# Performance work log

Hardware: AMD Instinct MI355X
Metric: run time of the kernel (lower is better)

Reference implementation:

```python
import jax, jax.numpy as jnp
import numpy as np

N = 50000      # nodes
E = 800000     # edges (before self loops)
EMB = 128      # input feature dim
HID = 32       # per-head hidden dim
HEADS = 4      # gat1 heads
G = 64         # graphs in batch
NEG_SLOPE = 0.2


def setup_inputs() -> dict:
    key = jax.random.key(0)
    ks = jax.random.split(key, 14)
    glorot = lambda k, shape, fan: (jax.random.normal(k, shape) / np.sqrt(fan)).astype(jnp.float32)
    x = jax.random.normal(ks[0], (N, EMB), dtype=jnp.float32)
    edge_index = jax.random.randint(ks[1], (2, E), 0, N, dtype=jnp.int64)
    batch = jnp.sort(jax.random.randint(ks[2], (N,), 0, G, dtype=jnp.int64))
    return {
        "x": x,
        "edge_index": edge_index,
        "batch": batch,
        # GATConv 1: EMB -> HID per head, HEADS heads, concat
        "W1": glorot(ks[3], (EMB, HEADS * HID), EMB),
        "att_src1": glorot(ks[4], (HEADS, HID), HID),
        "att_dst1": glorot(ks[5], (HEADS, HID), HID),
        "b1": jnp.zeros((HEADS * HID,), jnp.float32),
        # GATConv 2: HEADS*HID -> HID, 1 head
        "W2": glorot(ks[6], (HEADS * HID, HID), HEADS * HID),
        "att_src2": glorot(ks[7], (1, HID), HID),
        "att_dst2": glorot(ks[8], (1, HID), HID),
        "b2": jnp.zeros((HID,), jnp.float32),
        # attentional pooling gate MLP: Linear(HID,HID)->ReLU->Linear(HID,1)
        "g_w1": glorot(ks[9], (HID, HID), HID),
        "g_b1": jnp.zeros((HID,), jnp.float32),
        "g_w2": glorot(ks[10], (HID, 1), HID),
        "g_b2": jnp.zeros((1,), jnp.float32),
    }


def _gat(x, W, att_src, att_dst, bias, src, dst, heads, out_dim):
    """PyG-style GATConv with precomputed self-looped (src, dst)."""
    n = x.shape[0]
    h = (x @ W).reshape(n, heads, out_dim)              # [N, H, C]
    a_src = (h * att_src).sum(-1)                       # [N, H]
    a_dst = (h * att_dst).sum(-1)                       # [N, H]
    e = jax.nn.leaky_relu(a_src[src] + a_dst[dst], NEG_SLOPE)   # [Etot, H]
    # segment softmax over incoming edges of each dst node
    m = jax.ops.segment_max(e, dst, num_segments=n)
    ex = jnp.exp(e - m[dst])
    denom = jax.ops.segment_sum(ex, dst, num_segments=n)
    alpha = ex / (denom[dst] + 1e-16)                   # [Etot, H]
    out = jax.ops.segment_sum(alpha[:, :, None] * h[src], dst, num_segments=n)
    return out.reshape(n, heads * out_dim) + bias


def reference(x, edge_index, batch, W1, att_src1, att_dst1, b1,
              W2, att_src2, att_dst2, b2, g_w1, g_b1, g_w2, g_b2):
    n = x.shape[0]
    loops = jnp.arange(n, dtype=edge_index.dtype)
    src = jnp.concatenate([edge_index[0], loops])       # add_self_loops=True
    dst = jnp.concatenate([edge_index[1], loops])
    h = jax.nn.elu(_gat(x, W1, att_src1, att_dst1, b1, src, dst, HEADS, HID))
    h = jax.nn.elu(_gat(h, W2, att_src2, att_dst2, b2, src, dst, 1, HID))
    # attentional aggregation per graph
    gate = jax.nn.relu(h @ g_w1 + g_b1) @ g_w2 + g_b2   # [N, 1]
    gm = jax.ops.segment_max(gate, batch, num_segments=G)
    ge = jnp.exp(gate - gm[batch])
    gs = jax.ops.segment_sum(ge, batch, num_segments=G)
    w = ge / (gs[batch] + 1e-16)
    return jax.ops.segment_sum(w * h, batch, num_segments=G)  # [G, HID]
```

## Files before the change

kernel.cpp:

```cpp
#include <hip/hip_runtime.h>
#include <hip/hip_bf16.h>

#define NEG_SLOPE 0.2f
#define BW  128
#define BSH 7

__device__ __forceinline__ float elu1f(float v) {
    return v > 0.f ? v : expm1f(v);
}
__device__ __forceinline__ float bf2f(ushort u) {
    return __uint_as_float(((unsigned)u) << 16);
}
__device__ __forceinline__ ushort f2bf(float f) {
    return __bfloat16_as_ushort(__float2bfloat16(f));
}
__device__ __forceinline__ unsigned fflip(float f) {
    unsigned u = __float_as_uint(f);
    return (u & 0x80000000u) ? ~u : (u | 0x80000000u);
}
__device__ __forceinline__ float funflip(unsigned u) {
    u = (u & 0x80000000u) ? (u & 0x7FFFFFFFu) : ~u;
    return __uint_as_float(u);
}

__global__ __launch_bounds__(256) void k_bcount(
    const int* __restrict__ ei, int E, int Et, int nbk, int* __restrict__ bcnt)
{
    __shared__ int h[512];
    for (int i = threadIdx.x; i < nbk; i += 256) h[i] = 0;
    __syncthreads();
    const int start = blockIdx.x * 4096;
    const int end   = min(start + 4096, Et);
    for (int i = start + threadIdx.x; i < end; i += 256) {
        int d = (i < E) ? ei[E + i] : i - E;
        atomicAdd(&h[d >> BSH], 1);
    }
    __syncthreads();
    for (int i = threadIdx.x; i < nbk; i += 256)
        if (h[i]) atomicAdd(&bcnt[i], h[i]);
}

__global__ __launch_bounds__(512) void k_bscan(
    const int* __restrict__ bcnt, int nbk, int Et,
    int* __restrict__ bbase, int* __restrict__ bcur,
    const int* __restrict__ batch, int* __restrict__ gbound, int N, int G)
{
    __shared__ int s[512];
    int v = (threadIdx.x < nbk) ? bcnt[threadIdx.x] : 0;
    s[threadIdx.x] = v;
    __syncthreads();
#pragma unroll
    for (int off = 1; off < 512; off <<= 1) {
        int t = (threadIdx.x >= off) ? s[threadIdx.x - off] : 0;
        __syncthreads();
        s[threadIdx.x] += t;
        __syncthreads();
    }
    if (threadIdx.x < nbk) {
        int ex = s[threadIdx.x] - v;
        bbase[threadIdx.x] = ex;
        bcur[threadIdx.x]  = ex;
    }
    if (threadIdx.x == 0) bbase[nbk] = Et;
    if (threadIdx.x <= (unsigned)G) {
        int target = threadIdx.x;
        int lo = 0, hi = N;
        while (lo < hi) { int mid = (lo + hi) >> 1; if (batch[mid] < target) lo = mid + 1; else hi = mid; }
        gbound[threadIdx.x] = lo;
    }
}

__global__ __launch_bounds__(256) void k_bscatter(
    const int* __restrict__ ei, int E, int Et, int nbk,
    int* __restrict__ bcur, unsigned* __restrict__ ebuk)
{
    __shared__ int h[512];
    __shared__ int cur[512];
    for (int i = threadIdx.x; i < nbk; i += 256) h[i] = 0;
    __syncthreads();
    const int start = blockIdx.x * 4096;
    const int end   = min(start + 4096, Et);
    for (int i = start + threadIdx.x; i < end; i += 256) {
        int d = (i < E) ? ei[E + i] : i - E;
        atomicAdd(&h[d >> BSH], 1);
    }
    __syncthreads();
    for (int i = threadIdx.x; i < nbk; i += 256)
        cur[i] = h[i] ? atomicAdd(&bcur[i], h[i]) : 0;
    __syncthreads();
    for (int i = start + threadIdx.x; i < end; i += 256) {
        int s, d;
        if (i < E) { s = ei[i]; d = ei[E + i]; } else { s = i - E; d = s; }
        int p = atomicAdd(&cur[d >> BSH], 1);
        ebuk[p] = ((unsigned)(d & (BW - 1)) << 25) | (unsigned)s;
    }
}

__global__ __launch_bounds__(256) void k_csr(
    const unsigned* __restrict__ ebuk, const int* __restrict__ bbase,
    int N, int Et, int* __restrict__ rowp, int* __restrict__ esrc)
{
    const int b = blockIdx.x;
    __shared__ int cnt[BW];
    __shared__ int pre[BW];
    __shared__ int lcur[BW];
    if (threadIdx.x < BW) cnt[threadIdx.x] = 0;
    __syncthreads();
    const int e0 = bbase[b], e1 = bbase[b + 1];
    for (int i = e0 + threadIdx.x; i < e1; i += 256)
        atomicAdd(&cnt[ebuk[i] >> 25], 1);
    __syncthreads();
    if (threadIdx.x < BW) pre[threadIdx.x] = cnt[threadIdx.x];
    __syncthreads();
#pragma unroll
    for (int off = 1; off < BW; off <<= 1) {
        int v = (threadIdx.x < BW && threadIdx.x >= off) ? pre[threadIdx.x - off] : 0;
        __syncthreads();
        if (threadIdx.x < BW) pre[threadIdx.x] += v;
        __syncthreads();
    }
    const int d0 = b << BSH;
    if (threadIdx.x < BW) {
        int r = e0 + pre[threadIdx.x] - cnt[threadIdx.x];
        int d = d0 + threadIdx.x;
        if (d < N) rowp[d] = r;
        lcur[threadIdx.x] = r;
    }
    if (b == 0 && threadIdx.x == 0) rowp[N] = Et;
    __syncthreads();
    for (int i = e0 + threadIdx.x; i < e1; i += 256) {
        unsigned e = ebuk[i];
        int p = atomicAdd(&lcur[e >> 25], 1);
        esrc[p] = (int)(e & 0x1FFFFFFu);
    }
}

__global__ __launch_bounds__(256) void k_gemm1(
    const float* __restrict__ x, const float* __restrict__ W,
    const float* __restrict__ att_s, const float* __restrict__ att_d,
    ushort* __restrict__ h1, float* __restrict__ asT, float* __restrict__ ad1,
    unsigned* __restrict__ gmaxu, int N)
{
    __shared__ __align__(16) float sW[16][128];
    __shared__ __align__(16) float sX[32][16];
    __shared__ unsigned smax[4];
    const int t  = threadIdx.x;
    const int c4 = t & 31;
    const int rg = t >> 5;
    const int row0 = blockIdx.x * 32;
    const float4* W4 = (const float4*)W;

    if (t < 4) smax[t] = 0;

    float4 acc[4];
#pragma unroll
    for (int i = 0; i < 4; i++) acc[i] = {0.f, 0.f, 0.f, 0.f};

    for (int k0 = 0; k0 < 128; k0 += 16) {
        __syncthreads();
#pragma unroll
        for (int j = 0; j < 2; j++) {
            int idx = j * 256 + t;
            int r = idx >> 5, cc = idx & 31;
            *(float4*)&sW[r][cc * 4] = W4[(k0 + r) * 32 + cc];
        }
        if (t < 128) {
            int r = t >> 2, q = t & 3;
            int row = row0 + r;
            float4 v = {0.f, 0.f, 0.f, 0.f};
            if (row < N) v = *(const float4*)&x[(long long)row * 128 + k0 + q * 4];
            *(float4*)&sX[r][q * 4] = v;
        }
        __syncthreads();
#pragma unroll
        for (int g = 0; g < 4; g++) {
            const int kk = g * 4;
            const float4 w0 = *(const float4*)&sW[kk + 0][c4 * 4];
            const float4 w1 = *(const float4*)&sW[kk + 1][c4 * 4];
            const float4 w2 = *(const float4*)&sW[kk + 2][c4 * 4];
            const float4 w3 = *(const float4*)&sW[kk + 3][c4 * 4];
#pragma unroll
            for (int i = 0; i < 4; i++) {
                const float4 xv = *(const float4*)&sX[rg * 4 + i][kk];
                acc[i].x = fmaf(xv.x, w0.x, acc[i].x);
                acc[i].y = fmaf(xv.x, w0.y, acc[i].y);
                acc[i].z = fmaf(xv.x, w0.z, acc[i].z);
                acc[i].w = fmaf(xv.x, w0.w, acc[i].w);
                acc[i].x = fmaf(xv.y, w1.x, acc[i].x);
                acc[i].y = fmaf(xv.y, w1.y, acc[i].y);
                acc[i].z = fmaf(xv.y, w1.z, acc[i].z);
                acc[i].w = fmaf(xv.y, w1.w, acc[i].w);
                acc[i].x = fmaf(xv.z, w2.x, acc[i].x);
                acc[i].y = fmaf(xv.z, w2.y, acc[i].y);
                acc[i].z = fmaf(xv.z, w2.z, acc[i].z);
                acc[i].w = fmaf(xv.z, w2.w, acc[i].w);
                acc[i].x = fmaf(xv.w, w3.x, acc[i].x);
                acc[i].y = fmaf(xv.w, w3.y, acc[i].y);
                acc[i].z = fmaf(xv.w, w3.z, acc[i].z);
                acc[i].w = fmaf(xv.w, w3.w, acc[i].w);
            }
        }
    }

    const float4 avs = *(const float4*)&att_s[c4 * 4];
    const float4 avd = *(const float4*)&att_d[c4 * 4];
    const int hd = c4 >> 3;
    float lmax = -INFINITY;
#pragma unroll
    for (int i = 0; i < 4; i++) {
        int row = row0 + rg * 4 + i;
        if (row < N) {
            ushort4 hb;
            hb.x = f2bf(acc[i].x); hb.y = f2bf(acc[i].y);
            hb.z = f2bf(acc[i].z); hb.w = f2bf(acc[i].w);
            *(ushort4*)&h1[(long long)row * 128 + c4 * 4] = hb;
            float s = acc[i].x * avs.x + acc[i].y * avs.y + acc[i].z * avs.z + acc[i].w * avs.w;
            float d = acc[i].x * avd.x + acc[i].y * avd.y + acc[i].z * avd.z + acc[i].w * avd.w;
#pragma unroll
            for (int off = 4; off > 0; off >>= 1) {
                s += __shfl_xor(s, off, 64);
                d += __shfl_xor(d, off, 64);
            }
            if ((c4 & 7) == 0) {
                asT[(unsigned)hd * (unsigned)N + row] = s;
                ad1[row * 4 + hd] = d;
                lmax = fmaxf(lmax, s);
            }
        }
    }
    if ((c4 & 7) == 0) atomicMax(&smax[hd], fflip(lmax));
    __syncthreads();
    if (t < 4 && smax[t]) atomicMax(&gmaxu[t], smax[t]);
}

__global__ __launch_bounds__(256) void k_gemm2(
    const ushort* __restrict__ xin, const float* __restrict__ W,
    const float* __restrict__ b1,
    const float* __restrict__ att_s, const float* __restrict__ att_d,
    ushort* __restrict__ h2, float* __restrict__ as2, float* __restrict__ ad2,
    unsigned* __restrict__ gmax2u, int N)
{
    __shared__ __align__(16) float sW[16][32];
    __shared__ __align__(16) float sX[128][16];
    __shared__ unsigned smax1;
    const int t  = threadIdx.x;
    const int c4 = t & 7;
    const int rg = t >> 3;
    const int row0 = blockIdx.x * 128;
    const float4* W4 = (const float4*)W;

    if (t == 0) smax1 = 0;

    float4 acc[4];
#pragma unroll
    for (int i = 0; i < 4; i++) acc[i] = {0.f, 0.f, 0.f, 0.f};

    for (int k0 = 0; k0 < 128; k0 += 16) {
        __syncthreads();
        if (t < 128) {
            int r = t >> 3, cc = t & 7;
            *(float4*)&sW[r][cc * 4] = W4[(k0 + r) * 8 + cc];
        }
#pragma unroll
        for (int j = 0; j < 2; j++) {
            int idx = j * 256 + t;
            int r = idx >> 2, q = idx & 3;
            int row = row0 + r;
            float4 v = {0.f, 0.f, 0.f, 0.f};
            if (row < N) {
                const ushort4 uv = *(const ushort4*)&xin[(long long)row * 128 + k0 + q * 4];
                float4 b = *(const float4*)&b1[k0 + q * 4];
                v.x = elu1f(bf2f(uv.x) + b.x); v.y = elu1f(bf2f(uv.y) + b.y);
                v.z = elu1f(bf2f(uv.z) + b.z); v.w = elu1f(bf2f(uv.w) + b.w);
            }
            *(float4*)&sX[r][q * 4] = v;
        }
        __syncthreads();
#pragma unroll
        for (int g = 0; g < 4; g++) {
            const int kk = g * 4;
            const float4 w0 = *(const float4*)&sW[kk + 0][c4 * 4];
            const float4 w1 = *(const float4*)&sW[kk + 1][c4 * 4];
            const float4 w2 = *(const float4*)&sW[kk + 2][c4 * 4];
            const float4 w3 = *(const float4*)&sW[kk + 3][c4 * 4];
#pragma unroll
            for (int i = 0; i < 4; i++) {
                const float4 xv = *(const float4*)&sX[rg * 4 + i][kk];
                acc[i].x = fmaf(xv.x, w0.x, acc[i].x);
                acc[i].y = fmaf(xv.x, w0.y, acc[i].y);
                acc[i].z = fmaf(xv.x, w0.z, acc[i].z);
                acc[i].w = fmaf(xv.x, w0.w, acc[i].w);
                acc[i].x = fmaf(xv.y, w1.x, acc[i].x);
                acc[i].y = fmaf(xv.y, w1.y, acc[i].y);
                acc[i].z = fmaf(xv.y, w1.z, acc[i].z);
                acc[i].w = fmaf(xv.y, w1.w, acc[i].w);
                acc[i].x = fmaf(xv.z, w2.x, acc[i].x);
                acc[i].y = fmaf(xv.z, w2.y, acc[i].y);
                acc[i].z = fmaf(xv.z, w2.z, acc[i].z);
                acc[i].w = fmaf(xv.z, w2.w, acc[i].w);
                acc[i].x = fmaf(xv.w, w3.x, acc[i].x);
                acc[i].y = fmaf(xv.w, w3.y, acc[i].y);
                acc[i].z = fmaf(xv.w, w3.z, acc[i].z);
                acc[i].w = fmaf(xv.w, w3.w, acc[i].w);
            }
        }
    }

    const float4 avs = *(const float4*)&att_s[c4 * 4];
    const float4 avd = *(const float4*)&att_d[c4 * 4];
    float lmax = -INFINITY;
#pragma unroll
    for (int i = 0; i < 4; i++) {
        int row = row0 + rg * 4 + i;
        if (row < N) {
            ushort4 hb;
            hb.x = f2bf(acc[i].x); hb.y = f2bf(acc[i].y);
            hb.z = f2bf(acc[i].z); hb.w = f2bf(acc[i].w);
            *(ushort4*)&h2[(long long)row * 32 + c4 * 4] = hb;
            float s = acc[i].x * avs.x + acc[i].y * avs.y + acc[i].z * avs.z + acc[i].w * avs.w;
            float d = acc[i].x * avd.x + acc[i].y * avd.y + acc[i].z * avd.z + acc[i].w * avd.w;
#pragma unroll
            for (int off = 4; off > 0; off >>= 1) {
                s += __shfl_xor(s, off, 64);
                d += __shfl_xor(d, off, 64);
            }
            if (c4 == 0) {
                as2[row] = s; ad2[row] = d;
                lmax = fmaxf(lmax, s);
            }
        }
    }
    if (c4 == 0) atomicMax(&smax1, fflip(lmax));
    __syncthreads();
    if (t == 0 && smax1) atomicMax(&gmax2u[0], smax1);
}

__global__ __launch_bounds__(256) void k_agg1(
    const int* __restrict__ row, const int* __restrict__ esrc,
    const float* __restrict__ asT, const float* __restrict__ ad,
    const unsigned* __restrict__ gmaxu,
    const ushort* __restrict__ h,
    ushort* __restrict__ out, int N)
{
    const int lane = threadIdx.x & 63;
    const int wid  = threadIdx.x >> 6;
    const int n = blockIdx.x * 4 + wid;
    if (n >= N) return;
    const int e0 = row[n], e1 = row[n + 1];

    const float4 ad4 = *(const float4*)&ad[n * 4];
    const int half = lane >> 5;
    const int l    = lane & 31;
    const int hd   = l >> 3;
    const float adh = hd == 0 ? ad4.x : hd == 1 ? ad4.y : hd == 2 ? ad4.z : ad4.w;
    float mh = funflip(gmaxu[hd]) + adh;
    mh = mh >= 0.f ? mh : NEG_SLOPE * mh;

    const float* asH = asT + (unsigned)hd * (unsigned)N;
    const unsigned lofs = (unsigned)(l * 4);
    float4 acc = {0.f, 0.f, 0.f, 0.f};
    float wsum = 0.f;
    for (int base = e0; base < e1; base += 8) {
        const int eA = base + half,     eB = base + 2 + half;
        const int eC = base + 4 + half, eD = base + 6 + half;
        const bool vA = eA < e1, vB = eB < e1, vC = eC < e1, vD = eD < e1;
        const int sA = vA ? esrc[eA] : 0;
        const int sB = vB ? esrc[eB] : 0;
        const int sC = vC ? esrc[eC] : 0;
        const int sD = vD ? esrc[eD] : 0;
        const float aA = asH[sA];
        const float aB = asH[sB];
        const float aC = asH[sC];
        const float aD = asH[sD];
        const ushort4 hA = *(const ushort4*)&h[(unsigned)sA * 128u + lofs];
        const ushort4 hB = *(const ushort4*)&h[(unsigned)sB * 128u + lofs];
        const ushort4 hC = *(const ushort4*)&h[(unsigned)sC * 128u + lofs];
        const ushort4 hD = *(const ushort4*)&h[(unsigned)sD * 128u + lofs];

        float evA = aA + adh;
        evA = evA >= 0.f ? evA : NEG_SLOPE * evA;
        const float wA = vA ? __expf(evA - mh) : 0.f;
        float evB = aB + adh;
        evB = evB >= 0.f ? evB : NEG_SLOPE * evB;
        const float wB = vB ? __expf(evB - mh) : 0.f;
        float evC = aC + adh;
        evC = evC >= 0.f ? evC : NEG_SLOPE * evC;
        const float wC = vC ? __expf(evC - mh) : 0.f;
        float evD = aD + adh;
        evD = evD >= 0.f ? evD : NEG_SLOPE * evD;
        const float wD = vD ? __expf(evD - mh) : 0.f;

        acc.x = fmaf(wA, bf2f(hA.x), acc.x);
        acc.y = fmaf(wA, bf2f(hA.y), acc.y);
        acc.z = fmaf(wA, bf2f(hA.z), acc.z);
        acc.w = fmaf(wA, bf2f(hA.w), acc.w);
        acc.x = fmaf(wB, bf2f(hB.x), acc.x);
        acc.y = fmaf(wB, bf2f(hB.y), acc.y);
        acc.z = fmaf(wB, bf2f(hB.z), acc.z);
        acc.w = fmaf(wB, bf2f(hB.w), acc.w);
        acc.x = fmaf(wC, bf2f(hC.x), acc.x);
        acc.y = fmaf(wC, bf2f(hC.y), acc.y);
        acc.z = fmaf(wC, bf2f(hC.z), acc.z);
        acc.w = fmaf(wC, bf2f(hC.w), acc.w);
        acc.x = fmaf(wD, bf2f(hD.x), acc.x);
        acc.y = fmaf(wD, bf2f(hD.y), acc.y);
        acc.z = fmaf(wD, bf2f(hD.z), acc.z);
        acc.w = fmaf(wD, bf2f(hD.w), acc.w);
        wsum += (wA + wB) + (wC + wD);
    }
    acc.x += __shfl_xor(acc.x, 32, 64);
    acc.y += __shfl_xor(acc.y, 32, 64);
    acc.z += __shfl_xor(acc.z, 32, 64);
    acc.w += __shfl_xor(acc.w, 32, 64);
    wsum  += __shfl_xor(wsum, 32, 64);

    if (half == 0) {
        const float inv = 1.f / (wsum + 1e-16f);
        ushort4 ob;
        ob.x = f2bf(acc.x * inv); ob.y = f2bf(acc.y * inv);
        ob.z = f2bf(acc.z * inv); ob.w = f2bf(acc.w * inv);
        *(ushort4*)&out[(long long)n * 128 + l * 4] = ob;
    }
}

__global__ __launch_bounds__(256) void k_agg2(
    const int* __restrict__ row, const int* __restrict__ esrc,
    const float* __restrict__ as, const float* __restrict__ ad,
    const unsigned* __restrict__ gmax2u,
    const ushort* __restrict__ h,
    float* __restrict__ out, int N)
{
    const int lane = threadIdx.x & 63;
    const int wid  = threadIdx.x >> 6;
    const int n = blockIdx.x * 4 + wid;
    if (n >= N) return;
    const int e0 = row[n], e1 = row[n + 1];
    const float adv = ad[n];
    float m = funflip(gmax2u[0]) + adv;
    m = m >= 0.f ? m : NEG_SLOPE * m;

    const int g  = lane >> 3;
    const int l8 = lane & 7;
    const unsigned lofs = (unsigned)(l8 * 4);
    float4 acc = {0.f, 0.f, 0.f, 0.f};
    float wsum = 0.f;
    for (int base = e0; base < e1; base += 32) {
        const int eA = base + g,      eB = base + 8 + g;
        const int eC = base + 16 + g, eD = base + 24 + g;
        const bool vA = eA < e1, vB = eB < e1, vC = eC < e1, vD = eD < e1;
        const int sA = vA ? esrc[eA] : 0;
        const int sB = vB ? esrc[eB] : 0;
        const int sC = vC ? esrc[eC] : 0;
        const int sD = vD ? esrc[eD] : 0;
        const float asA = as[sA], asB = as[sB], asC = as[sC], asD = as[sD];
        const ushort4 hA = *(const ushort4*)&h[(unsigned)sA * 32u + lofs];
        const ushort4 hB = *(const ushort4*)&h[(unsigned)sB * 32u + lofs];
        const ushort4 hC = *(const ushort4*)&h[(unsigned)sC * 32u + lofs];
        const ushort4 hD = *(const ushort4*)&h[(unsigned)sD * 32u + lofs];

        float evA = asA + adv; evA = evA >= 0.f ? evA : NEG_SLOPE * evA;
        const float wA = vA ? __expf(evA - m) : 0.f;
        float evB = asB + adv; evB = evB >= 0.f ? evB : NEG_SLOPE * evB;
        const float wB = vB ? __expf(evB - m) : 0.f;
        float evC = asC + adv; evC = evC >= 0.f ? evC : NEG_SLOPE * evC;
        const float wC = vC ? __expf(evC - m) : 0.f;
        float evD = asD + adv; evD = evD >= 0.f ? evD : NEG_SLOPE * evD;
        const float wD = vD ? __expf(evD - m) : 0.f;

        acc.x = fmaf(wA, bf2f(hA.x), acc.x);
        acc.y = fmaf(wA, bf2f(hA.y), acc.y);
        acc.z = fmaf(wA, bf2f(hA.z), acc.z);
        acc.w = fmaf(wA, bf2f(hA.w), acc.w);
        acc.x = fmaf(wB, bf2f(hB.x), acc.x);
        acc.y = fmaf(wB, bf2f(hB.y), acc.y);
        acc.z = fmaf(wB, bf2f(hB.z), acc.z);
        acc.w = fmaf(wB, bf2f(hB.w), acc.w);
        acc.x = fmaf(wC, bf2f(hC.x), acc.x);
        acc.y = fmaf(wC, bf2f(hC.y), acc.y);
        acc.z = fmaf(wC, bf2f(hC.z), acc.z);
        acc.w = fmaf(wC, bf2f(hC.w), acc.w);
        acc.x = fmaf(wD, bf2f(hD.x), acc.x);
        acc.y = fmaf(wD, bf2f(hD.y), acc.y);
        acc.z = fmaf(wD, bf2f(hD.z), acc.z);
        acc.w = fmaf(wD, bf2f(hD.w), acc.w);
        wsum += (wA + wB) + (wC + wD);
    }
#pragma unroll
    for (int off = 8; off < 64; off <<= 1) {
        acc.x += __shfl_xor(acc.x, off, 64);
        acc.y += __shfl_xor(acc.y, off, 64);
        acc.z += __shfl_xor(acc.z, off, 64);
        acc.w += __shfl_xor(acc.w, off, 64);
        wsum  += __shfl_xor(wsum, off, 64);
    }
    if (lane < 8) {
        const float inv = 1.f / (wsum + 1e-16f);
        float4 o; o.x = acc.x * inv; o.y = acc.y * inv; o.z = acc.z * inv; o.w = acc.w * inv;
        *(float4*)&out[(long long)n * 32 + lane * 4] = o;
    }
}

__global__ __launch_bounds__(256) void k_gate(
    const float* __restrict__ out2, const float* __restrict__ b2,
    const float* __restrict__ gw1, const float* __restrict__ gb1,
    const float* __restrict__ gw2, const float* __restrict__ gb2,
    float* __restrict__ gate, int N)
{
    const int c = threadIdx.x & 31, grp = threadIdx.x >> 5;
    const int n = blockIdx.x * 8 + grp;
    if (n >= N) return;
    float v = out2[(long long)n * 32 + c] + b2[c];
    v = elu1f(v);
    float t1 = gb1[c];
#pragma unroll
    for (int k = 0; k < 32; k++) {
        float hk = __shfl(v, k, 32);
        t1 = fmaf(hk, gw1[k * 32 + c], t1);
    }
    t1 = fmaxf(t1, 0.f);
    float gv = t1 * gw2[c];
#pragma unroll
    for (int off = 16; off > 0; off >>= 1) gv += __shfl_xor(gv, off, 32);
    if (c == 0) gate[n] = gv + gb2[0];
}

__global__ __launch_bounds__(256) void k_gmax(
    const float* __restrict__ gate, const int* __restrict__ gbound,
    unsigned* __restrict__ gmax)
{
    const int g  = blockIdx.x >> 3;
    const int ch = blockIdx.x & 7;
    const int s0 = gbound[g], s1 = gbound[g + 1];
    const int len = s1 - s0;
    const int c0 = s0 + (int)(((long long)len * ch) >> 3);
    const int c1 = s0 + (int)(((long long)len * (ch + 1)) >> 3);

    __shared__ float sred[4];
    float m = -INFINITY;
    for (int n = c0 + threadIdx.x; n < c1; n += 256) m = fmaxf(m, gate[n]);
#pragma unroll
    for (int off = 32; off > 0; off >>= 1) m = fmaxf(m, __shfl_xor(m, off, 64));
    if ((threadIdx.x & 63) == 0) sred[threadIdx.x >> 6] = m;
    __syncthreads();
    if (threadIdx.x == 0) {
        m = fmaxf(fmaxf(sred[0], sred[1]), fmaxf(sred[2], sred[3]));
        atomicMax(&gmax[g], fflip(m));
    }
}

__global__ __launch_bounds__(256) void k_pool3(
    const float* __restrict__ out2, const float* __restrict__ b2,
    const float* __restrict__ gate, const int* __restrict__ gbound,
    const unsigned* __restrict__ gmax, float* __restrict__ partials)
{
    const int g  = blockIdx.x >> 3;
    const int ch = blockIdx.x & 7;
    const int s0 = gbound[g], s1 = gbound[g + 1];
    const int len = s1 - s0;
    const int c0 = s0 + (int)(((long long)len * ch) >> 3);
    const int c1 = s0 + (int)(((long long)len * (ch + 1)) >> 3);

    const int c   = threadIdx.x & 31;
    const int grp = threadIdx.x >> 5;
    const float gm = funflip(gmax[g]);
    const float bc = b2[c];

    __shared__ float sacc[8][32];
    __shared__ float swsum[8];

    float acc = 0.f, wsum = 0.f;
    for (int n = c0 + grp; n < c1; n += 8) {
        float v = elu1f(out2[(long long)n * 32 + c] + bc);
        float ge = __expf(gate[n] - gm);
        acc = fmaf(ge, v, acc);
        wsum += ge;
    }
    sacc[grp][c] = acc;
    if (c == 0) swsum[grp] = wsum;
    __syncthreads();

    if (grp == 0) {
        float a = 0.f, wtot = 0.f;
#pragma unroll
        for (int i = 0; i < 8; i++) { a += sacc[i][c]; wtot += swsum[i]; }
        partials[(long long)blockIdx.x * 33 + c] = a;
        if (c == 0) partials[(long long)blockIdx.x * 33 + 32] = wtot;
    }
}

__global__ __launch_bounds__(256) void k_pool4(
    const float* __restrict__ partials, float* __restrict__ out)
{
    const int g   = blockIdx.x;
    const int c   = threadIdx.x & 31;
    const int p   = threadIdx.x >> 5;

    __shared__ float sacc[8][32];
    __shared__ float swsum[8];

    sacc[p][c] = partials[(long long)(g * 8 + p) * 33 + c];
    if (c == 0) swsum[p] = partials[(long long)(g * 8 + p) * 33 + 32];
    __syncthreads();

    if (p == 0) {
        float a = 0.f, wtot = 0.f;
#pragma unroll
        for (int i = 0; i < 8; i++) { a += sacc[i][c]; wtot += swsum[i]; }
        out[g * 32 + c] = a / (wtot + 1e-16f);
    }
}

extern "C" void kernel_launch(void* const* d_in, const int* in_sizes, int n_in,
                              void* d_out, int out_size, void* d_ws, size_t ws_size,
                              hipStream_t stream)
{
    const float* x    = (const float*)d_in[0];
    const int*   ei   = (const int*)d_in[1];
    const int*   batch= (const int*)d_in[2];
    const float* W1   = (const float*)d_in[3];
    const float* as1w = (const float*)d_in[4];
    const float* ad1w = (const float*)d_in[5];
    const float* b1   = (const float*)d_in[6];
    const float* W2   = (const float*)d_in[7];
    const float* as2w = (const float*)d_in[8];
    const float* ad2w = (const float*)d_in[9];
    const float* b2   = (const float*)d_in[10];
    const float* gw1  = (const float*)d_in[11];
    const float* gb1  = (const float*)d_in[12];
    const float* gw2  = (const float*)d_in[13];
    const float* gb2  = (const float*)d_in[14];

    const int N  = in_sizes[2];
    const int E  = in_sizes[1] / 2;
    const int Et = E + N;
    const int G  = 64;
    const int nbk   = (N + BW - 1) >> BSH;
    const int nchk  = (Et + 4095) / 4096;
    const int nblk1 = (N + 31) / 32;
    const int nblk2 = (N + 127) / 128;

    float* ws = (float*)d_ws;
    size_t o = 0;
    unsigned* ebuk = (unsigned*)(ws + o); o += (size_t)Et * 2;
    ushort* h1 = (ushort*)(ws + o); o += (size_t)N * 64;
    ushort* out1 = (ushort*)(ws + o); o += (size_t)N * 64;
    ushort* h2 = (ushort*)(ws + o); o += (size_t)N * 16;
    float* out2 = ws + o; o += (size_t)N * 32;
    float* asT1 = ws + o; o += (size_t)N * 4;
    float* a_d1 = ws + o; o += (size_t)N * 4;
    float* a_s2 = ws + o; o += (size_t)N;
    float* a_d2 = ws + o; o += (size_t)N;
    float* gate = ws + o; o += (size_t)N;
    int*   rowp = (int*)(ws + o); o += (size_t)N + 1;
    int*   esrc = (int*)(ws + o); o += (size_t)Et;
    int*   bbase= (int*)(ws + o); o += (size_t)nbk + 1;
    int*   bcur = (int*)(ws + o); o += (size_t)nbk;
    int*   gbound = (int*)(ws + o); o += G + 1;
    float* partials = ws + o; o += (size_t)G * 8 * 33;
    size_t zstart = o;
    int*      bcnt   = (int*)(ws + o); o += (size_t)nbk;
    unsigned* gmax   = (unsigned*)(ws + o); o += G;
    unsigned* gmaxu  = (unsigned*)(ws + o); o += 4;
    unsigned* gmax2u = (unsigned*)(ws + o); o += 4;
    size_t zbytes = (o - zstart) * sizeof(float);

    hipMemsetAsync(ws + zstart, 0, zbytes, stream);

    k_bcount  <<<nchk, 256, 0, stream>>>(ei, E, Et, nbk, bcnt);
    k_bscan   <<<1, 512, 0, stream>>>(bcnt, nbk, Et, bbase, bcur, batch, gbound, N, G);
    k_bscatter<<<nchk, 256, 0, stream>>>(ei, E, Et, nbk, bcur, ebuk);
    k_csr     <<<nbk, 256, 0, stream>>>(ebuk, bbase, N, Et, rowp, esrc);

    k_gemm1<<<nblk1, 256, 0, stream>>>(x, W1, as1w, ad1w, h1, asT1, a_d1, gmaxu, N);
    k_agg1 <<<(N + 3) / 4, 256, 0, stream>>>(rowp, esrc, asT1, a_d1, gmaxu, h1, out1, N);

    k_gemm2<<<nblk2, 256, 0, stream>>>(out1, W2, b1, as2w, ad2w, h2, a_s2, a_d2, gmax2u, N);
    k_agg2 <<<(N + 3) / 4, 256, 0, stream>>>(rowp, esrc, a_s2, a_d2, gmax2u, h2, out2, N);

    k_gate <<<(N + 7) / 8, 256, 0, stream>>>(out2, b2, gw1, gb1, gw2, gb2, gate, N);
    k_gmax <<<G * 8, 256, 0, stream>>>(gate, gbound, gmax);
    k_pool3<<<G * 8, 256, 0, stream>>>(out2, b2, gate, gbound, gmax, partials);
    k_pool4<<<G, 256, 0, stream>>>(partials, (float*)d_out);
}
```

Before: 205.4 us.

## Fuse gate MLP and global gate max into second GAT aggregation kernel

Folds the gate MLP (ELU, Linear, ReLU, Linear) into the tail of k_agg2 so it works on the aggregated row while still in registers. This removes the k_gate launch and its reread of out2. It also replaces the per-graph max kernel k_gmax with a single global max, reduced through 8 atomic slots, which k_pool3 then uses as the softmax shift. Using one global max instead of one per graph is mathematically equivalent, but it risks underflow for graphs whose gates sit far below the global maximum.

```diff
diff --git a/kernel.cpp b/kernel.cpp
--- a/kernel.cpp
+++ b/kernel.cpp
@@ -428,14 +428,22 @@
     const float* __restrict__ as, const float* __restrict__ ad,
     const unsigned* __restrict__ gmax2u,
     const ushort* __restrict__ h,
-    float* __restrict__ out, int N)
-{
+    const float* __restrict__ b2,
+    const float* __restrict__ gw1, const float* __restrict__ gb1,
+    const float* __restrict__ gw2, const float* __restrict__ gb2,
+    float* __restrict__ out, float* __restrict__ gate,
+    unsigned* __restrict__ gGu, int N)
+{
+    __shared__ unsigned sgmax;
     const int lane = threadIdx.x & 63;
     const int wid  = threadIdx.x >> 6;
     const int n = blockIdx.x * 4 + wid;
-    if (n >= N) return;
-    const int e0 = row[n], e1 = row[n + 1];
-    const float adv = ad[n];
+    const bool valid = n < N;
+    if (threadIdx.x == 0) sgmax = 0;
+
+    const int e0 = valid ? row[n] : 0;
+    const int e1 = valid ? row[n + 1] : 0;
+    const float adv = valid ? ad[n] : 0.f;
     float m = funflip(gmax2u[0]) + adv;
     m = m >= 0.f ? m : NEG_SLOPE * m;
 
@@ -493,40 +501,46 @@
         acc.w += __shfl_xor(acc.w, off, 64);
         wsum  += __shfl_xor(wsum, off, 64);
     }
-    if (lane < 8) {
-        const float inv = 1.f / (wsum + 1e-16f);
-        float4 o; o.x = acc.x * inv; o.y = acc.y * inv; o.z = acc.z * inv; o.w = acc.w * inv;
+    const float inv = 1.f / (wsum + 1e-16f);
+    float4 o; o.x = acc.x * inv; o.y = acc.y * inv; o.z = acc.z * inv; o.w = acc.w * inv;
+    if (valid && lane < 8) {
         *(float4*)&out[(long long)n * 32 + lane * 4] = o;
     }
-}
-
-__global__ __launch_bounds__(256) void k_gate(
-    const float* __restrict__ out2, const float* __restrict__ b2,
-    const float* __restrict__ gw1, const float* __restrict__ gb1,
-    const float* __restrict__ gw2, const float* __restrict__ gb2,
-    float* __restrict__ gate, int N)
-{
-    const int c = threadIdx.x & 31, grp = threadIdx.x >> 5;
-    const int n = blockIdx.x * 8 + grp;
-    if (n >= N) return;
-    float v = out2[(long long)n * 32 + c] + b2[c];
-    v = elu1f(v);
+
+    float4 eo;
+    eo.x = elu1f(o.x + b2[l8 * 4 + 0]);
+    eo.y = elu1f(o.y + b2[l8 * 4 + 1]);
+    eo.z = elu1f(o.z + b2[l8 * 4 + 2]);
+    eo.w = elu1f(o.w + b2[l8 * 4 + 3]);
+    const int c = lane & 31;
     float t1 = gb1[c];
 #pragma unroll
     for (int k = 0; k < 32; k++) {
-        float hk = __shfl(v, k, 32);
+        float comp;
+        if ((k & 3) == 0) comp = eo.x;
+        else if ((k & 3) == 1) comp = eo.y;
+        else if ((k & 3) == 2) comp = eo.z;
+        else comp = eo.w;
+        float hk = __shfl(comp, k >> 2, 64);
         t1 = fmaf(hk, gw1[k * 32 + c], t1);
     }
     t1 = fmaxf(t1, 0.f);
     float gv = t1 * gw2[c];
 #pragma unroll
     for (int off = 16; off > 0; off >>= 1) gv += __shfl_xor(gv, off, 32);
-    if (c == 0) gate[n] = gv + gb2[0];
-}
-
-__global__ __launch_bounds__(256) void k_gmax(
+    const float gval = gv + gb2[0];
+    if (valid && lane == 0) {
+        gate[n] = gval;
+        atomicMax(&sgmax, fflip(gval));
+    }
+    __syncthreads();
+    if (threadIdx.x == 0 && sgmax) atomicMax(&gGu[blockIdx.x & 7], sgmax);
+}
+
+__global__ __launch_bounds__(256) void k_pool3(
+    const float* __restrict__ out2, const float* __restrict__ b2,
     const float* __restrict__ gate, const int* __restrict__ gbound,
-    unsigned* __restrict__ gmax)
+    const unsigned* __restrict__ gGu, float* __restrict__ partials)
 {
     const int g  = blockIdx.x >> 3;
     const int ch = blockIdx.x & 7;
@@ -535,34 +549,13 @@
     const int c0 = s0 + (int)(((long long)len * ch) >> 3);
     const int c1 = s0 + (int)(((long long)len * (ch + 1)) >> 3);
 
-    __shared__ float sred[4];
-    float m = -INFINITY;
-    for (int n = c0 + threadIdx.x; n < c1; n += 256) m = fmaxf(m, gate[n]);
-#pragma unroll
-    for (int off = 32; off > 0; off >>= 1) m = fmaxf(m, __shfl_xor(m, off, 64));
-    if ((threadIdx.x & 63) == 0) sred[threadIdx.x >> 6] = m;
-    __syncthreads();
-    if (threadIdx.x == 0) {
-        m = fmaxf(fmaxf(sred[0], sred[1]), fmaxf(sred[2], sred[3]));
-        atomicMax(&gmax[g], fflip(m));
-    }
-}
-
-__global__ __launch_bounds__(256) void k_pool3(
-    const float* __restrict__ out2, const float* __restrict__ b2,
-    const float* __restrict__ gate, const int* __restrict__ gbound,
-    const unsigned* __restrict__ gmax, float* __restrict__ partials)
-{
-    const int g  = blockIdx.x >> 3;
-    const int ch = blockIdx.x & 7;
-    const int s0 = gbound[g], s1 = gbound[g + 1];
-    const int len = s1 - s0;
-    const int c0 = s0 + (int)(((long long)len * ch) >> 3);
-    const int c1 = s0 + (int)(((long long)len * (ch + 1)) >> 3);
+    unsigned mu = gGu[0];
+#pragma unroll
+    for (int i = 1; i < 8; i++) mu = max(mu, gGu[i]);
+    const float gm = funflip(mu);
 
     const int c   = threadIdx.x & 31;
     const int grp = threadIdx.x >> 5;
-    const float gm = funflip(gmax[g]);
     const float bc = b2[c];
 
     __shared__ float sacc[8][32];
@@ -659,9 +652,9 @@
     float* partials = ws + o; o += (size_t)G * 8 * 33;
     size_t zstart = o;
     int*      bcnt   = (int*)(ws + o); o += (size_t)nbk;
-    unsigned* gmax   = (unsigned*)(ws + o); o += G;
     unsigned* gmaxu  = (unsigned*)(ws + o); o += 4;
     unsigned* gmax2u = (unsigned*)(ws + o); o += 4;
+    unsigned* gGu    = (unsigned*)(ws + o); o += 8;
     size_t zbytes = (o - zstart) * sizeof(float);
 
     hipMemsetAsync(ws + zstart, 0, zbytes, stream);
@@ -675,10 +668,9 @@
     k_agg1 <<<(N + 3) / 4, 256, 0, stream>>>(rowp, esrc, asT1, a_d1, gmaxu, h1, out1, N);
 
     k_gemm2<<<nblk2, 256, 0, stream>>>(out1, W2, b1, as2w, ad2w, h2, a_s2, a_d2, gmax2u, N);
-    k_agg2 <<<(N + 3) / 4, 256, 0, stream>>>(rowp, esrc, a_s2, a_d2, gmax2u, h2, out2, N);
-
-    k_gate <<<(N + 7) / 8, 256, 0, stream>>>(out2, b2, gw1, gb1, gw2, gb2, gate, N);
-    k_gmax <<<G * 8, 256, 0, stream>>>(gate, gbound, gmax);
-    k_pool3<<<G * 8, 256, 0, stream>>>(out2, b2, gate, gbound, gmax, partials);
+    k_agg2 <<<(N + 3) / 4, 256, 0, stream>>>(rowp, esrc, a_s2, a_d2, gmax2u, h2,
+                                             b2, gw1, gb1, gw2, gb2, out2, gate, gGu, N);
+
+    k_pool3<<<G * 8, 256, 0, stream>>>(out2, b2, gate, gbound, gGu, partials);
     k_pool4<<<G, 256, 0, stream>>>(partials, (float*)d_out);
 }
```

New measurement: 319.8 us. 55.7% more time.
